# Kernel optimization log

Measured on AMD Instinct MI355X. Metric: run time of the kernel, lower is better.

The kernel has to match this reference:

```python
import jax, jax.numpy as jnp
import numpy as np

B, IN, OUT, E, H, K = 8192, 1024, 256, 16, 512, 3
EPS = 1e-10


def setup_inputs() -> dict:
    key = jax.random.key(0)
    ks = jax.random.split(key, 5)
    scaled = lambda k, shape, fan: jax.random.normal(k, shape, jnp.float32) / np.sqrt(fan)
    return {
        "x": jax.random.normal(ks[0], (B, IN), jnp.float32),
        # torch init is zeros for w_gate (degenerate ties); use small random for a meaningful reference
        "w_gate": jax.random.normal(ks[1], (IN, E), jnp.float32) * 0.02,
        "W1": scaled(ks[2], (E, IN, H), IN),
        "b1": jnp.zeros((E, H), jnp.float32),
        "W2": scaled(ks[3], (E, H, OUT), H),
        "b2": jnp.zeros((E, OUT), jnp.float32),
    }


def _cv_squared(v):
    # torch .var() is unbiased (ddof=1)
    return jnp.var(v, ddof=1) / (jnp.mean(v) ** 2 + EPS)


def reference(x, w_gate, W1, b1, W2, b2):
    # --- top-k gating (eval mode: clean logits, no noise) ---
    logits = x @ w_gate                                   # [B, E]
    top_vals, top_idx = jax.lax.top_k(logits, K)          # [B, K]
    top_gates = jax.nn.softmax(top_vals, axis=-1)         # softmax over selected k
    rows = jnp.arange(logits.shape[0])[:, None]
    gates = jnp.zeros_like(logits).at[rows, top_idx].set(top_gates)  # sparse gates [B, E]

    # --- load-balancing loss ---
    importance = gates.sum(0)
    load = (gates > 0).sum(0).astype(jnp.float32)         # _gates_to_load (eval path)
    loss = _cv_squared(importance) + _cv_squared(load)

    # --- experts (MLP stand-in; dense compute, sparse combine via zero gates) ---
    h = jax.nn.relu(jnp.einsum('bi,eih->beh', x, W1) + b1)  # [B, E, H]
    expert_out = jnp.einsum('beh,eho->beo', h, W2) + b2     # [B, E, OUT]

    # combine: equivalent to SparseDispatcher gather/split/scatter-add with gate weighting
    y = jnp.einsum('be,beo->bo', gates, expert_out)         # [B, OUT]
    return y, loss
```

## Files before the change

kernel.cpp:

```cpp
#include <hip/hip_runtime.h>

#define B_ 8192
#define IN_ 1024
#define OUT_ 256
#define E_ 16
#define KTOP 3
#define H_ 512
#define MAXSLOTS 26624
#define NTILES 208
#define HBLK 16
#define GBLK 2048

typedef __bf16 bf16;
typedef __bf16 bf16x4 __attribute__((ext_vector_type(4)));
typedef __bf16 bf16x8 __attribute__((ext_vector_type(8)));
typedef float f32x4 __attribute__((ext_vector_type(4)));

__device__ __forceinline__ void async16(const bf16* g, bf16* l) {
    __builtin_amdgcn_global_load_lds(
        (const __attribute__((address_space(1))) void*)g,
        (__attribute__((address_space(3))) void*)l,
        16, 0, 0);
}

__global__ __launch_bounds__(256) void k_setup(
    const float* __restrict__ W1, bf16* __restrict__ w1t,
    const float* __restrict__ W2, bf16* __restrict__ w2t,
    int* __restrict__ row_ids, const float* __restrict__ wg, float* __restrict__ wgT,
    bf16* __restrict__ zero_row, int* __restrict__ tile_expert) {
    int bx = blockIdx.x;
    int t = threadIdx.x;
    if (bx >= 2560) {
        if (bx < 2664) {
            row_ids[(bx - 2560) * 256 + t] = -1;
        } else if (bx < 2728) {
            int id = (bx - 2664) * 256 + t;
            int e = id >> 10, j = id & 1023;
            wgT[id] = wg[j * E_ + e];
        } else {
#pragma unroll
            for (int i = 0; i < 4; i++) zero_row[t * 4 + i] = (bf16)0.f;
            if (t < NTILES) tile_expert[t] = -1;
        }
        return;
    }
    __shared__ float tile[64][65];
    const float* in; bf16* out; int Kd, Nd, e, tk, tn;
    if (bx < 2048) {
        in = W1; out = w1t; Kd = IN_; Nd = H_;
        e = bx >> 7; int tt = bx & 127; tk = tt >> 3; tn = tt & 7;
    } else {
        int b2x = bx - 2048;
        in = W2; out = w2t; Kd = H_; Nd = OUT_;
        e = b2x >> 5; int tt = b2x & 31; tk = tt >> 2; tn = tt & 3;
    }
    int r = t >> 6, c = t & 63;
    const float* src = in + ((size_t)e * Kd + tk * 64) * Nd + (size_t)tn * 64;
#pragma unroll
    for (int i = 0; i < 16; i++) {
        int rr = r + i * 4;
        tile[rr][c] = src[(size_t)rr * Nd + c];
    }
    __syncthreads();
    bf16* dst = out + ((size_t)e * Nd + tn * 64) * Kd + (size_t)tk * 64;
#pragma unroll
    for (int i = 0; i < 16; i++) {
        int rr = r + i * 4;
        dst[(size_t)rr * Kd + c] = (bf16)tile[c][rr];
    }
}

__global__ __launch_bounds__(256) void k_gating(
    const float* __restrict__ x, const float* __restrict__ wgT,
    bf16* __restrict__ xbf, int* __restrict__ top_idx, float* __restrict__ top_gate,
    int* __restrict__ partial) {
    __shared__ int lcnt[16];
    int t = threadIdx.x;
    int row = blockIdx.x * 4 + (t >> 6);
    int lane = t & 63;
    if (t < 16) lcnt[t] = 0;
    __syncthreads();
    float acc[16];
#pragma unroll
    for (int e = 0; e < 16; e++) acc[e] = 0.f;
    const float4* x4p = (const float4*)(x + (size_t)row * IN_);
    const float4* w4 = (const float4*)wgT;
#pragma unroll
    for (int it = 0; it < 4; it++) {
        int j0 = it * 64 + lane;
        float4 xv = x4p[j0];
        bf16x4 xb;
        xb[0] = (bf16)xv.x; xb[1] = (bf16)xv.y; xb[2] = (bf16)xv.z; xb[3] = (bf16)xv.w;
        *(bf16x4*)(xbf + (size_t)row * IN_ + j0 * 4) = xb;
#pragma unroll
        for (int e = 0; e < 16; e++) {
            float4 wv = w4[e * 256 + j0];
            acc[e] += xv.x * wv.x + xv.y * wv.y + xv.z * wv.z + xv.w * wv.w;
        }
    }
#pragma unroll
    for (int e = 0; e < 16; e++) {
#pragma unroll
        for (int s = 32; s > 0; s >>= 1) acc[e] += __shfl_xor(acc[e], s, 64);
    }
    if (lane == 0) {
        float v[16];
#pragma unroll
        for (int e = 0; e < 16; e++) v[e] = acc[e];
        int idx[KTOP];
        float val[KTOP];
#pragma unroll
        for (int k = 0; k < KTOP; k++) {
            int best = 0;
            float bv = v[0];
            for (int e = 1; e < 16; e++) {
                if (v[e] > bv) { bv = v[e]; best = e; }
            }
            idx[k] = best; val[k] = bv; v[best] = -1e30f;
        }
        float e1 = __expf(val[1] - val[0]);
        float e2 = __expf(val[2] - val[0]);
        float inv = 1.f / (1.f + e1 + e2);
        float g[KTOP] = {inv, e1 * inv, e2 * inv};
#pragma unroll
        for (int k = 0; k < KTOP; k++) {
            top_idx[row * KTOP + k] = idx[k];
            top_gate[row * KTOP + k] = g[k];
            atomicAdd(&lcnt[idx[k]], 1);
        }
    }
    __syncthreads();
    if (t < 16) partial[blockIdx.x * 16 + t] = lcnt[t];
}

__global__ __launch_bounds__(256) void k_scatterscan(
    const int* __restrict__ top_idx, const float* __restrict__ top_gate,
    const int* __restrict__ partial,
    int* __restrict__ counts, int* __restrict__ tile_expert,
    int* __restrict__ row_ids, int* __restrict__ rowslot,
    float* __restrict__ partial_imp) {
    __shared__ int segsum[16][16];
    __shared__ int tote[16];
    __shared__ int sbase[16];
    __shared__ int lcnt[16];
    __shared__ float limp[16];
    int t = threadIdx.x;
    int blk = blockIdx.x;
    int e = t & 15, seg = t >> 4;
    int s = 0;
    for (int i = 0; i < 128; i++) s += partial[(seg * 128 + i) * 16 + e];
    segsum[seg][e] = s;
    if (t < 16) { lcnt[t] = 0; limp[t] = 0.f; }
    __syncthreads();
    if (t < 16) {
        int total = 0, pre = 0;
        for (int sg = 0; sg < 16; sg++) {
            int v = segsum[sg][t];
            total += v;
            if (sg < blk) pre += v;
        }
        tote[t] = total;
        segsum[0][t] = pre;
    }
    __syncthreads();
    if (t < 16) {
        int off = 0;
        for (int ee = 0; ee < 16; ee++) {
            if (ee == t) break;
            off += (tote[ee] + 127) & ~127;
        }
        sbase[t] = off + segsum[0][t];
        if (blk == 0) {
            counts[t] = tote[t];
            int pd = (tote[t] + 127) & ~127;
            for (int tt = off >> 7; tt < (off + pd) >> 7; ++tt) tile_expert[tt] = t;
        }
    }
    __syncthreads();
#pragma unroll
    for (int j = 0; j < 6; j++) {
        int gid = blk * 1536 + j * 256 + t;
        int ee = top_idx[gid];
        float g = top_gate[gid];
        int rank = atomicAdd(&lcnt[ee], 1);
        atomicAdd(&limp[ee], g);
        int slot = sbase[ee] + rank;
        row_ids[slot] = gid / KTOP;
        rowslot[gid] = slot;
    }
    __syncthreads();
    if (t < 16) partial_imp[blk * 16 + t] = limp[t];
}

__global__ __launch_bounds__(256) void k_gemm1(
    const bf16* __restrict__ xbf, const bf16* __restrict__ w1t,
    const float* __restrict__ b1, const int* __restrict__ row_ids,
    const int* __restrict__ tile_expert, const bf16* __restrict__ zero_row,
    bf16* __restrict__ h) {
    int e = tile_expert[blockIdx.y];
    if (e < 0) return;
    int slot_base = blockIdx.y * 128;
    int nbase = blockIdx.x * 128;
    __shared__ __align__(16) bf16 As[128 * 64];
    __shared__ __align__(16) bf16 Bs[128 * 64];
    int t = threadIdx.x;
    int rmod = (t >> 3) & 7;
    int cglob = (t & 7) ^ rmod;
    const bf16* gA[4];
    const bf16* gB[4];
#pragma unroll
    for (int j = 0; j < 4; j++) {
        int m = j * 32 + (t >> 3);
        int rid = row_ids[slot_base + m];
        gA[j] = ((rid >= 0) ? xbf + (size_t)rid * IN_ : zero_row) + cglob * 8;
        gB[j] = w1t + ((size_t)e * H_ + nbase + m) * IN_ + cglob * 8;
    }
    int w = t >> 6, lane = t & 63;
    int wm = (w >> 1) * 64, wn = (w & 1) * 64;
    int lm = lane & 15, lq = lane >> 4;
    f32x4 acc[4][4] = {};
    for (int k0 = 0; k0 < IN_; k0 += 64) {
#pragma unroll
        for (int j = 0; j < 4; j++) {
            async16(gA[j] + k0, As + (j * 256 + t) * 8);
            async16(gB[j] + k0, Bs + (j * 256 + t) * 8);
        }
        __syncthreads();
        const bf16x8* Av = (const bf16x8*)As;
        const bf16x8* Bv = (const bf16x8*)Bs;
#pragma unroll
        for (int ks = 0; ks < 2; ks++) {
            int kc = ks * 4 + lq;
            bf16x8 af[4], bfv[4];
#pragma unroll
            for (int i = 0; i < 4; i++) {
                int row = wm + i * 16 + lm;
                af[i] = Av[row * 8 + (kc ^ (row & 7))];
            }
#pragma unroll
            for (int i = 0; i < 4; i++) {
                int row = wn + i * 16 + lm;
                bfv[i] = Bv[row * 8 + (kc ^ (row & 7))];
            }
#pragma unroll
            for (int mi = 0; mi < 4; mi++)
#pragma unroll
                for (int ni = 0; ni < 4; ni++)
                    acc[mi][ni] = __builtin_amdgcn_mfma_f32_16x16x32_bf16(af[mi], bfv[ni], acc[mi][ni], 0, 0, 0);
        }
        __syncthreads();
    }
#pragma unroll
    for (int mi = 0; mi < 4; mi++) {
#pragma unroll
        for (int ni = 0; ni < 4; ni++) {
            int colg = nbase + wn + ni * 16 + lm;
            float bias = b1[e * H_ + colg];
#pragma unroll
            for (int r = 0; r < 4; r++) {
                int rowl = wm + mi * 16 + lq * 4 + r;
                float v = acc[mi][ni][r] + bias;
                v = v > 0.f ? v : 0.f;
                h[(size_t)(slot_base + rowl) * H_ + colg] = (bf16)v;
            }
        }
    }
}

__global__ __launch_bounds__(256) void k_gemm2(
    const bf16* __restrict__ h, const bf16* __restrict__ w2t,
    const float* __restrict__ b2, const int* __restrict__ tile_expert,
    bf16* __restrict__ eout) {
    int e = tile_expert[blockIdx.x];
    if (e < 0) return;
    int slot_base = blockIdx.x * 128;
    __shared__ __align__(16) bf16 As[128 * 64];
    __shared__ __align__(16) bf16 Bs[256 * 64];
    int t = threadIdx.x;
    int rmod = (t >> 3) & 7;
    int cglob = (t & 7) ^ rmod;
    const bf16* gA[4];
    const bf16* gB[8];
#pragma unroll
    for (int j = 0; j < 4; j++) {
        int m = j * 32 + (t >> 3);
        gA[j] = h + (size_t)(slot_base + m) * H_ + cglob * 8;
    }
#pragma unroll
    for (int j = 0; j < 8; j++) {
        int m = j * 32 + (t >> 3);
        gB[j] = w2t + ((size_t)e * OUT_ + m) * H_ + cglob * 8;
    }
    int w = t >> 6, lane = t & 63;
    int wm = (w >> 1) * 64, wn = (w & 1) * 128;
    int lm = lane & 15, lq = lane >> 4;
    f32x4 acc[4][8] = {};
    for (int k0 = 0; k0 < H_; k0 += 64) {
#pragma unroll
        for (int j = 0; j < 4; j++) async16(gA[j] + k0, As + (j * 256 + t) * 8);
#pragma unroll
        for (int j = 0; j < 8; j++) async16(gB[j] + k0, Bs + (j * 256 + t) * 8);
        __syncthreads();
        const bf16x8* Av = (const bf16x8*)As;
        const bf16x8* Bv = (const bf16x8*)Bs;
#pragma unroll
        for (int ks = 0; ks < 2; ks++) {
            int kc = ks * 4 + lq;
            bf16x8 af[4], bfv[8];
#pragma unroll
            for (int i = 0; i < 4; i++) {
                int row = wm + i * 16 + lm;
                af[i] = Av[row * 8 + (kc ^ (row & 7))];
            }
#pragma unroll
            for (int i = 0; i < 8; i++) {
                int row = wn + i * 16 + lm;
                bfv[i] = Bv[row * 8 + (kc ^ (row & 7))];
            }
#pragma unroll
            for (int mi = 0; mi < 4; mi++)
#pragma unroll
                for (int ni = 0; ni < 8; ni++)
                    acc[mi][ni] = __builtin_amdgcn_mfma_f32_16x16x32_bf16(af[mi], bfv[ni], acc[mi][ni], 0, 0, 0);
        }
        __syncthreads();
    }
#pragma unroll
    for (int mi = 0; mi < 4; mi++) {
#pragma unroll
        for (int ni = 0; ni < 8; ni++) {
            int colg = wn + ni * 16 + lm;
            float bias = b2[e * OUT_ + colg];
#pragma unroll
            for (int r = 0; r < 4; r++) {
                int rowl = wm + mi * 16 + lq * 4 + r;
                eout[(size_t)(slot_base + rowl) * OUT_ + colg] = (bf16)(acc[mi][ni][r] + bias);
            }
        }
    }
}

__global__ __launch_bounds__(256) void k_combine(
    const bf16* __restrict__ eout, const int* __restrict__ rowslot,
    const float* __restrict__ top_gate, float* __restrict__ y,
    const float* __restrict__ partial_imp, const int* __restrict__ counts,
    float* __restrict__ loss_out) {
    int t = threadIdx.x;
    if (blockIdx.x == B_ / 4) {
        __shared__ float imp[16];
        if (t < 16) {
            float s = 0.f;
#pragma unroll
            for (int b = 0; b < HBLK; b++) s += partial_imp[b * 16 + t];
            imp[t] = s;
        }
        __syncthreads();
        if (t == 0) {
            float si = 0.f, sl = 0.f;
            for (int e = 0; e < E_; e++) { si += imp[e]; sl += (float)counts[e]; }
            float mi_ = si / (float)E_, ml_ = sl / (float)E_;
            float vi = 0.f, vl = 0.f;
            for (int e = 0; e < E_; e++) {
                float d = imp[e] - mi_; vi += d * d;
                float d2 = (float)counts[e] - ml_; vl += d2 * d2;
            }
            vi /= (float)(E_ - 1); vl /= (float)(E_ - 1);
            *loss_out = vi / (mi_ * mi_ + 1e-10f) + vl / (ml_ * ml_ + 1e-10f);
        }
        return;
    }
    int b = blockIdx.x * 4 + (t >> 6);
    int lane = t & 63;
    int s0 = rowslot[b * 3], s1 = rowslot[b * 3 + 1], s2 = rowslot[b * 3 + 2];
    float g0 = top_gate[b * 3], g1 = top_gate[b * 3 + 1], g2 = top_gate[b * 3 + 2];
    bf16x4 v0 = *(const bf16x4*)(eout + (size_t)s0 * OUT_ + lane * 4);
    bf16x4 v1 = *(const bf16x4*)(eout + (size_t)s1 * OUT_ + lane * 4);
    bf16x4 v2 = *(const bf16x4*)(eout + (size_t)s2 * OUT_ + lane * 4);
    float4 r;
    r.x = g0 * (float)v0[0] + g1 * (float)v1[0] + g2 * (float)v2[0];
    r.y = g0 * (float)v0[1] + g1 * (float)v1[1] + g2 * (float)v2[1];
    r.z = g0 * (float)v0[2] + g1 * (float)v1[2] + g2 * (float)v2[2];
    r.w = g0 * (float)v0[3] + g1 * (float)v1[3] + g2 * (float)v2[3];
    ((float4*)y)[(size_t)b * 64 + lane] = r;
}

extern "C" void kernel_launch(void* const* d_in, const int* in_sizes, int n_in,
                              void* d_out, int out_size, void* d_ws, size_t ws_size,
                              hipStream_t stream) {
    (void)in_sizes; (void)n_in; (void)out_size; (void)ws_size;
    const float* x = (const float*)d_in[0];
    const float* wgate = (const float*)d_in[1];
    const float* W1 = (const float*)d_in[2];
    const float* b1 = (const float*)d_in[3];
    const float* W2 = (const float*)d_in[4];
    const float* b2 = (const float*)d_in[5];
    float* y = (float*)d_out;

    char* p = (char*)d_ws;
    auto alloc = [&](size_t bytes) {
        char* q = p;
        p += (bytes + 255) & ~(size_t)255;
        return q;
    };
    bf16* xbf = (bf16*)alloc((size_t)B_ * IN_ * 2);
    bf16* w1t = (bf16*)alloc((size_t)E_ * H_ * IN_ * 2);
    bf16* w2t = (bf16*)alloc((size_t)E_ * OUT_ * H_ * 2);
    bf16* h = (bf16*)alloc((size_t)MAXSLOTS * H_ * 2);
    int* row_ids = (int*)alloc((size_t)MAXSLOTS * 4);
    int* rowslot = (int*)alloc((size_t)B_ * KTOP * 4);
    int* top_idx = (int*)alloc((size_t)B_ * KTOP * 4);
    float* top_gate = (float*)alloc((size_t)B_ * KTOP * 4);
    int* counts = (int*)alloc(E_ * 4);
    int* partial = (int*)alloc((size_t)GBLK * E_ * 4);
    float* partial_imp = (float*)alloc(HBLK * E_ * 4);
    int* tile_expert = (int*)alloc(NTILES * 4);
    bf16* zero_row = (bf16*)alloc(IN_ * 2);
    float* wgT = (float*)alloc((size_t)E_ * IN_ * 4);
    bf16* eout = (bf16*)xbf;

    k_setup<<<dim3(2729), dim3(256), 0, stream>>>(
        W1, w1t, W2, w2t, row_ids, wgate, wgT, zero_row, tile_expert);
    k_gating<<<dim3(GBLK), dim3(256), 0, stream>>>(x, wgT, xbf, top_idx, top_gate, partial);
    k_scatterscan<<<dim3(HBLK), dim3(256), 0, stream>>>(
        top_idx, top_gate, partial, counts, tile_expert, row_ids, rowslot, partial_imp);
    k_gemm1<<<dim3(H_ / 128, NTILES), dim3(256), 0, stream>>>(
        xbf, w1t, b1, row_ids, tile_expert, zero_row, h);
    k_gemm2<<<dim3(NTILES), dim3(256), 0, stream>>>(
        h, w2t, b2, tile_expert, eout);
    k_combine<<<dim3(B_ / 4 + 1), dim3(256), 0, stream>>>(
        eout, rowslot, top_gate, y, partial_imp, counts, y + (size_t)B_ * OUT_);
}
```

Baseline: 212.4 us.

## Fuse MoE pipeline into one persistent kernel with software grid barriers

Replaces the six separate launches (setup, gating, scatter/scan, two expert GEMMs, combine) with a single persistent kernel of 512 blocks. The stages are separated by hand-written atomic grid barriers, plus a tiny kernel that zeroes the barrier counters. Gating now stages w_gate through LDS instead of a pre-transposed copy, and row_ids padding is cleared per expert instead of in full. This is meant to remove launch gaps and tail effects between stages. In exchange it depends on all 512 blocks being co-resident (two per CU) and pays spin-barrier costs, and fewer blocks may underfill the GEMM stages.

Result: slower. 581.2 us (+173.6%).

```diff
diff --git a/kernel.cpp b/kernel.cpp
--- a/kernel.cpp
+++ b/kernel.cpp
@@ -8,8 +8,9 @@
 #define H_ 512
 #define MAXSLOTS 26624
 #define NTILES 208
-#define HBLK 16
-#define GBLK 2048
+#define NBLK 512
+#define GUNITS 2048
+#define P0UNITS 4609
 
 typedef __bf16 bf16;
 typedef __bf16 bf16x4 __attribute__((ext_vector_type(4)));
@@ -23,365 +24,411 @@
         16, 0, 0);
 }
 
-__global__ __launch_bounds__(256) void k_setup(
-    const float* __restrict__ W1, bf16* __restrict__ w1t,
-    const float* __restrict__ W2, bf16* __restrict__ w2t,
-    int* __restrict__ row_ids, const float* __restrict__ wg, float* __restrict__ wgT,
-    bf16* __restrict__ zero_row, int* __restrict__ tile_expert) {
-    int bx = blockIdx.x;
+__global__ void k_zero(int* __restrict__ bar) {
+    for (int i = threadIdx.x; i < 4 * 17 * 32; i += 256) bar[i] = 0;
+}
+
+__device__ __forceinline__ void gbar(int* bar, int b, int blk) {
+    __syncthreads();
+    if (threadIdx.x == 0) {
+        int* base = bar + b * 17 * 32;
+        __threadfence();
+        __hip_atomic_fetch_add(base + (blk & 15) * 32, 1, __ATOMIC_RELEASE, __HIP_MEMORY_SCOPE_AGENT);
+        if (blk == 0) {
+            int sum;
+            do {
+                sum = 0;
+                for (int i = 0; i < 16; i++)
+                    sum += __hip_atomic_load(base + i * 32, __ATOMIC_RELAXED, __HIP_MEMORY_SCOPE_AGENT);
+                if (sum < NBLK) __builtin_amdgcn_s_sleep(8);
+            } while (sum < NBLK);
+            __hip_atomic_store(base + 16 * 32, 1, __ATOMIC_RELEASE, __HIP_MEMORY_SCOPE_AGENT);
+        } else {
+            while (__hip_atomic_load(base + 16 * 32, __ATOMIC_ACQUIRE, __HIP_MEMORY_SCOPE_AGENT) == 0)
+                __builtin_amdgcn_s_sleep(8);
+        }
+        __threadfence();
+    }
+    __syncthreads();
+}
+
+__global__ __launch_bounds__(256, 2) void k_mega(
+    const float* __restrict__ x, const float* __restrict__ wg,
+    const float* __restrict__ W1, const float* __restrict__ b1,
+    const float* __restrict__ W2, const float* __restrict__ b2,
+    bf16* __restrict__ xbf, bf16* __restrict__ w1t, bf16* __restrict__ w2t,
+    bf16* __restrict__ h, bf16* __restrict__ eout,
+    int* __restrict__ row_ids, int* __restrict__ rowslot,
+    int* __restrict__ top_idx, float* __restrict__ top_gate,
+    int* __restrict__ counts, int* __restrict__ partial,
+    float* __restrict__ partial_imp, int* __restrict__ tile_expert,
+    bf16* __restrict__ zero_row, float* __restrict__ y, float* __restrict__ loss_out,
+    int* __restrict__ bar) {
+    __shared__ __align__(16) char smem[49152];
+    int blk = blockIdx.x;
     int t = threadIdx.x;
-    if (bx >= 2560) {
-        if (bx < 2664) {
-            row_ids[(bx - 2560) * 256 + t] = -1;
-        } else if (bx < 2728) {
-            int id = (bx - 2664) * 256 + t;
-            int e = id >> 10, j = id & 1023;
-            wgT[id] = wg[j * E_ + e];
+    int lane = t & 63;
+
+    for (int u = blk; u < P0UNITS; u += NBLK) {
+        if (u < GUNITS) {
+            float4* swg4 = (float4*)smem;
+            int* lcnt = (int*)(smem + 20480);
+            int row = u * 4 + (t >> 6);
+            if (t < 16) lcnt[t] = 0;
+            __syncthreads();
+            float acc[16];
+#pragma unroll
+            for (int e = 0; e < 16; e++) acc[e] = 0.f;
+            const float4* x4p = (const float4*)(x + (size_t)row * IN_);
+            for (int q = 0; q < 4; q++) {
+                const float4* src = (const float4*)(wg + q * 4096);
+#pragma unroll
+                for (int i = 0; i < 4; i++) {
+                    int f = i * 256 + t;
+                    swg4[(f >> 2) * 5 + (f & 3)] = src[f];
+                }
+                __syncthreads();
+                float4 xv = x4p[q * 64 + lane];
+                bf16x4 xb;
+                xb[0] = (bf16)xv.x; xb[1] = (bf16)xv.y; xb[2] = (bf16)xv.z; xb[3] = (bf16)xv.w;
+                *(bf16x4*)(xbf + (size_t)row * IN_ + (q * 64 + lane) * 4) = xb;
+                float xs[4] = {xv.x, xv.y, xv.z, xv.w};
+#pragma unroll
+                for (int i = 0; i < 4; i++) {
+                    int r = lane * 4 + i;
+#pragma unroll
+                    for (int e4 = 0; e4 < 4; e4++) {
+                        float4 wv = swg4[r * 5 + e4];
+                        acc[e4 * 4 + 0] += xs[i] * wv.x;
+                        acc[e4 * 4 + 1] += xs[i] * wv.y;
+                        acc[e4 * 4 + 2] += xs[i] * wv.z;
+                        acc[e4 * 4 + 3] += xs[i] * wv.w;
+                    }
+                }
+                __syncthreads();
+            }
+#pragma unroll
+            for (int e = 0; e < 16; e++) {
+#pragma unroll
+                for (int s = 32; s > 0; s >>= 1) acc[e] += __shfl_xor(acc[e], s, 64);
+            }
+            if (lane == 0) {
+                float v[16];
+#pragma unroll
+                for (int e = 0; e < 16; e++) v[e] = acc[e];
+                int idx[KTOP];
+                float val[KTOP];
+#pragma unroll
+                for (int k = 0; k < KTOP; k++) {
+                    int best = 0;
+                    float bv = v[0];
+                    for (int e = 1; e < 16; e++) {
+                        if (v[e] > bv) { bv = v[e]; best = e; }
+                    }
+                    idx[k] = best; val[k] = bv; v[best] = -1e30f;
+                }
+                float e1 = __expf(val[1] - val[0]);
+                float e2 = __expf(val[2] - val[0]);
+                float inv = 1.f / (1.f + e1 + e2);
+                float g[KTOP] = {inv, e1 * inv, e2 * inv};
+#pragma unroll
+                for (int k = 0; k < KTOP; k++) {
+                    top_idx[row * KTOP + k] = idx[k];
+                    top_gate[row * KTOP + k] = g[k];
+                    atomicAdd(&lcnt[idx[k]], 1);
+                }
+            }
+            __syncthreads();
+            if (t < 16) partial[u * 16 + t] = lcnt[t];
+        } else if (u < 4608) {
+            __syncthreads();
+            float (*tile)[65] = (float(*)[65])smem;
+            const float* in; bf16* out; int Kd, Nd, e, tk, tn;
+            if (u < 4096) {
+                int b1x = u - 2048;
+                in = W1; out = w1t; Kd = IN_; Nd = H_;
+                e = b1x >> 7; int tt = b1x & 127; tk = tt >> 3; tn = tt & 7;
+            } else {
+                int b2x = u - 4096;
+                in = W2; out = w2t; Kd = H_; Nd = OUT_;
+                e = b2x >> 5; int tt = b2x & 31; tk = tt >> 2; tn = tt & 3;
+            }
+            int r = t >> 6, c = t & 63;
+            const float* src = in + ((size_t)e * Kd + tk * 64) * Nd + (size_t)tn * 64;
+#pragma unroll
+            for (int i = 0; i < 16; i++) {
+                int rr = r + i * 4;
+                tile[rr][c] = src[(size_t)rr * Nd + c];
+            }
+            __syncthreads();
+            bf16* dst = out + ((size_t)e * Nd + tn * 64) * Kd + (size_t)tk * 64;
+#pragma unroll
+            for (int i = 0; i < 16; i++) {
+                int rr = r + i * 4;
+                dst[(size_t)rr * Kd + c] = (bf16)tile[c][rr];
+            }
         } else {
 #pragma unroll
             for (int i = 0; i < 4; i++) zero_row[t * 4 + i] = (bf16)0.f;
-            if (t < NTILES) tile_expert[t] = -1;
-        }
-        return;
-    }
-    __shared__ float tile[64][65];
-    const float* in; bf16* out; int Kd, Nd, e, tk, tn;
-    if (bx < 2048) {
-        in = W1; out = w1t; Kd = IN_; Nd = H_;
-        e = bx >> 7; int tt = bx & 127; tk = tt >> 3; tn = tt & 7;
-    } else {
-        int b2x = bx - 2048;
-        in = W2; out = w2t; Kd = H_; Nd = OUT_;
-        e = b2x >> 5; int tt = b2x & 31; tk = tt >> 2; tn = tt & 3;
-    }
-    int r = t >> 6, c = t & 63;
-    const float* src = in + ((size_t)e * Kd + tk * 64) * Nd + (size_t)tn * 64;
-#pragma unroll
-    for (int i = 0; i < 16; i++) {
-        int rr = r + i * 4;
-        tile[rr][c] = src[(size_t)rr * Nd + c];
-    }
-    __syncthreads();
-    bf16* dst = out + ((size_t)e * Nd + tn * 64) * Kd + (size_t)tk * 64;
-#pragma unroll
-    for (int i = 0; i < 16; i++) {
-        int rr = r + i * 4;
-        dst[(size_t)rr * Kd + c] = (bf16)tile[c][rr];
-    }
-}
-
-__global__ __launch_bounds__(256) void k_gating(
-    const float* __restrict__ x, const float* __restrict__ wgT,
-    bf16* __restrict__ xbf, int* __restrict__ top_idx, float* __restrict__ top_gate,
-    int* __restrict__ partial) {
-    __shared__ int lcnt[16];
-    int t = threadIdx.x;
-    int row = blockIdx.x * 4 + (t >> 6);
-    int lane = t & 63;
-    if (t < 16) lcnt[t] = 0;
-    __syncthreads();
-    float acc[16];
-#pragma unroll
-    for (int e = 0; e < 16; e++) acc[e] = 0.f;
-    const float4* x4p = (const float4*)(x + (size_t)row * IN_);
-    const float4* w4 = (const float4*)wgT;
-#pragma unroll
-    for (int it = 0; it < 4; it++) {
-        int j0 = it * 64 + lane;
-        float4 xv = x4p[j0];
-        bf16x4 xb;
-        xb[0] = (bf16)xv.x; xb[1] = (bf16)xv.y; xb[2] = (bf16)xv.z; xb[3] = (bf16)xv.w;
-        *(bf16x4*)(xbf + (size_t)row * IN_ + j0 * 4) = xb;
-#pragma unroll
-        for (int e = 0; e < 16; e++) {
-            float4 wv = w4[e * 256 + j0];
-            acc[e] += xv.x * wv.x + xv.y * wv.y + xv.z * wv.z + xv.w * wv.w;
-        }
-    }
-#pragma unroll
-    for (int e = 0; e < 16; e++) {
-#pragma unroll
-        for (int s = 32; s > 0; s >>= 1) acc[e] += __shfl_xor(acc[e], s, 64);
-    }
-    if (lane == 0) {
-        float v[16];
-#pragma unroll
-        for (int e = 0; e < 16; e++) v[e] = acc[e];
-        int idx[KTOP];
-        float val[KTOP];
-#pragma unroll
-        for (int k = 0; k < KTOP; k++) {
-            int best = 0;
-            float bv = v[0];
-            for (int e = 1; e < 16; e++) {
-                if (v[e] > bv) { bv = v[e]; best = e; }
-            }
-            idx[k] = best; val[k] = bv; v[best] = -1e30f;
-        }
-        float e1 = __expf(val[1] - val[0]);
-        float e2 = __expf(val[2] - val[0]);
-        float inv = 1.f / (1.f + e1 + e2);
-        float g[KTOP] = {inv, e1 * inv, e2 * inv};
-#pragma unroll
-        for (int k = 0; k < KTOP; k++) {
-            top_idx[row * KTOP + k] = idx[k];
-            top_gate[row * KTOP + k] = g[k];
-            atomicAdd(&lcnt[idx[k]], 1);
-        }
-    }
-    __syncthreads();
-    if (t < 16) partial[blockIdx.x * 16 + t] = lcnt[t];
-}
-
-__global__ __launch_bounds__(256) void k_scatterscan(
-    const int* __restrict__ top_idx, const float* __restrict__ top_gate,
-    const int* __restrict__ partial,
-    int* __restrict__ counts, int* __restrict__ tile_expert,
-    int* __restrict__ row_ids, int* __restrict__ rowslot,
-    float* __restrict__ partial_imp) {
-    __shared__ int segsum[16][16];
-    __shared__ int tote[16];
-    __shared__ int sbase[16];
-    __shared__ int lcnt[16];
-    __shared__ float limp[16];
-    int t = threadIdx.x;
-    int blk = blockIdx.x;
-    int e = t & 15, seg = t >> 4;
-    int s = 0;
-    for (int i = 0; i < 128; i++) s += partial[(seg * 128 + i) * 16 + e];
-    segsum[seg][e] = s;
-    if (t < 16) { lcnt[t] = 0; limp[t] = 0.f; }
-    __syncthreads();
-    if (t < 16) {
-        int total = 0, pre = 0;
-        for (int sg = 0; sg < 16; sg++) {
-            int v = segsum[sg][t];
-            total += v;
-            if (sg < blk) pre += v;
-        }
-        tote[t] = total;
-        segsum[0][t] = pre;
-    }
-    __syncthreads();
-    if (t < 16) {
-        int off = 0;
-        for (int ee = 0; ee < 16; ee++) {
-            if (ee == t) break;
-            off += (tote[ee] + 127) & ~127;
-        }
-        sbase[t] = off + segsum[0][t];
+        }
+    }
+    gbar(bar, 0, blk);
+
+    if (blk < 16) {
+        struct SS {
+            int segsum[16][16];
+            int tote[16], spre[16], soff[16], lcnt[16];
+            float limp[16];
+        };
+        SS* ss = (SS*)smem;
+        int e = t & 15, seg = t >> 4;
+        int s = 0;
+        for (int i = 0; i < 128; i++) s += partial[(seg * 128 + i) * 16 + e];
+        ss->segsum[seg][e] = s;
+        if (t < 16) { ss->lcnt[t] = 0; ss->limp[t] = 0.f; }
+        __syncthreads();
+        if (t < 16) {
+            int total = 0, pre = 0;
+            for (int sg = 0; sg < 16; sg++) {
+                int v = ss->segsum[sg][t];
+                total += v;
+                if (sg < blk) pre += v;
+            }
+            ss->tote[t] = total;
+            ss->spre[t] = pre;
+        }
+        __syncthreads();
+        if (t < 16) {
+            int off = 0;
+            for (int ee = 0; ee < t; ee++) off += (ss->tote[ee] + 127) & ~127;
+            ss->soff[t] = off;
+            if (blk == 0) counts[t] = ss->tote[t];
+        }
+        __syncthreads();
         if (blk == 0) {
-            counts[t] = tote[t];
-            int pd = (tote[t] + 127) & ~127;
-            for (int tt = off >> 7; tt < (off + pd) >> 7; ++tt) tile_expert[tt] = t;
-        }
-    }
-    __syncthreads();
-#pragma unroll
-    for (int j = 0; j < 6; j++) {
-        int gid = blk * 1536 + j * 256 + t;
-        int ee = top_idx[gid];
-        float g = top_gate[gid];
-        int rank = atomicAdd(&lcnt[ee], 1);
-        atomicAdd(&limp[ee], g);
-        int slot = sbase[ee] + rank;
-        row_ids[slot] = gid / KTOP;
-        rowslot[gid] = slot;
-    }
-    __syncthreads();
-    if (t < 16) partial_imp[blk * 16 + t] = limp[t];
-}
-
-__global__ __launch_bounds__(256) void k_gemm1(
-    const bf16* __restrict__ xbf, const bf16* __restrict__ w1t,
-    const float* __restrict__ b1, const int* __restrict__ row_ids,
-    const int* __restrict__ tile_expert, const bf16* __restrict__ zero_row,
-    bf16* __restrict__ h) {
-    int e = tile_expert[blockIdx.y];
-    if (e < 0) return;
-    int slot_base = blockIdx.y * 128;
-    int nbase = blockIdx.x * 128;
-    __shared__ __align__(16) bf16 As[128 * 64];
-    __shared__ __align__(16) bf16 Bs[128 * 64];
-    int t = threadIdx.x;
-    int rmod = (t >> 3) & 7;
-    int cglob = (t & 7) ^ rmod;
-    const bf16* gA[4];
-    const bf16* gB[4];
-#pragma unroll
-    for (int j = 0; j < 4; j++) {
-        int m = j * 32 + (t >> 3);
-        int rid = row_ids[slot_base + m];
-        gA[j] = ((rid >= 0) ? xbf + (size_t)rid * IN_ : zero_row) + cglob * 8;
-        gB[j] = w1t + ((size_t)e * H_ + nbase + m) * IN_ + cglob * 8;
-    }
-    int w = t >> 6, lane = t & 63;
-    int wm = (w >> 1) * 64, wn = (w & 1) * 64;
-    int lm = lane & 15, lq = lane >> 4;
-    f32x4 acc[4][4] = {};
-    for (int k0 = 0; k0 < IN_; k0 += 64) {
-#pragma unroll
-        for (int j = 0; j < 4; j++) {
-            async16(gA[j] + k0, As + (j * 256 + t) * 8);
-            async16(gB[j] + k0, Bs + (j * 256 + t) * 8);
+            if (t < 16) {
+                int off = ss->soff[t], pd = (ss->tote[t] + 127) & ~127;
+                for (int tt = off >> 7; tt < (off + pd) >> 7; ++tt) tile_expert[tt] = t;
+            }
+            if (t == 0) {
+                int tot = ss->soff[15] + ((ss->tote[15] + 127) & ~127);
+                for (int tt = tot >> 7; tt < NTILES; ++tt) tile_expert[tt] = -1;
+            }
+        }
+        {
+            int pb = ss->soff[blk] + ss->tote[blk];
+            int pe = ss->soff[blk] + ((ss->tote[blk] + 127) & ~127);
+            for (int i = pb + t; i < pe; i += 256) row_ids[i] = -1;
+        }
+#pragma unroll
+        for (int j = 0; j < 6; j++) {
+            int gid = blk * 1536 + j * 256 + t;
+            int ee = top_idx[gid];
+            float g = top_gate[gid];
+            int rank = atomicAdd(&ss->lcnt[ee], 1);
+            atomicAdd(&ss->limp[ee], g);
+            int slot = ss->soff[ee] + ss->spre[ee] + rank;
+            row_ids[slot] = gid / KTOP;
+            rowslot[gid] = slot;
         }
         __syncthreads();
-        const bf16x8* Av = (const bf16x8*)As;
-        const bf16x8* Bv = (const bf16x8*)Bs;
-#pragma unroll
-        for (int ks = 0; ks < 2; ks++) {
-            int kc = ks * 4 + lq;
-            bf16x8 af[4], bfv[4];
-#pragma unroll
-            for (int i = 0; i < 4; i++) {
-                int row = wm + i * 16 + lm;
-                af[i] = Av[row * 8 + (kc ^ (row & 7))];
-            }
-#pragma unroll
-            for (int i = 0; i < 4; i++) {
-                int row = wn + i * 16 + lm;
-                bfv[i] = Bv[row * 8 + (kc ^ (row & 7))];
-            }
-#pragma unroll
-            for (int mi = 0; mi < 4; mi++)
-#pragma unroll
-                for (int ni = 0; ni < 4; ni++)
-                    acc[mi][ni] = __builtin_amdgcn_mfma_f32_16x16x32_bf16(af[mi], bfv[ni], acc[mi][ni], 0, 0, 0);
-        }
-        __syncthreads();
-    }
-#pragma unroll
-    for (int mi = 0; mi < 4; mi++) {
-#pragma unroll
-        for (int ni = 0; ni < 4; ni++) {
-            int colg = nbase + wn + ni * 16 + lm;
-            float bias = b1[e * H_ + colg];
-#pragma unroll
-            for (int r = 0; r < 4; r++) {
-                int rowl = wm + mi * 16 + lq * 4 + r;
-                float v = acc[mi][ni][r] + bias;
-                v = v > 0.f ? v : 0.f;
-                h[(size_t)(slot_base + rowl) * H_ + colg] = (bf16)v;
-            }
-        }
-    }
-}
-
-__global__ __launch_bounds__(256) void k_gemm2(
-    const bf16* __restrict__ h, const bf16* __restrict__ w2t,
-    const float* __restrict__ b2, const int* __restrict__ tile_expert,
-    bf16* __restrict__ eout) {
-    int e = tile_expert[blockIdx.x];
-    if (e < 0) return;
-    int slot_base = blockIdx.x * 128;
-    __shared__ __align__(16) bf16 As[128 * 64];
-    __shared__ __align__(16) bf16 Bs[256 * 64];
-    int t = threadIdx.x;
-    int rmod = (t >> 3) & 7;
-    int cglob = (t & 7) ^ rmod;
-    const bf16* gA[4];
-    const bf16* gB[8];
-#pragma unroll
-    for (int j = 0; j < 4; j++) {
-        int m = j * 32 + (t >> 3);
-        gA[j] = h + (size_t)(slot_base + m) * H_ + cglob * 8;
-    }
-#pragma unroll
-    for (int j = 0; j < 8; j++) {
-        int m = j * 32 + (t >> 3);
-        gB[j] = w2t + ((size_t)e * OUT_ + m) * H_ + cglob * 8;
-    }
-    int w = t >> 6, lane = t & 63;
-    int wm = (w >> 1) * 64, wn = (w & 1) * 128;
-    int lm = lane & 15, lq = lane >> 4;
-    f32x4 acc[4][8] = {};
-    for (int k0 = 0; k0 < H_; k0 += 64) {
-#pragma unroll
-        for (int j = 0; j < 4; j++) async16(gA[j] + k0, As + (j * 256 + t) * 8);
-#pragma unroll
-        for (int j = 0; j < 8; j++) async16(gB[j] + k0, Bs + (j * 256 + t) * 8);
-        __syncthreads();
-        const bf16x8* Av = (const bf16x8*)As;
-        const bf16x8* Bv = (const bf16x8*)Bs;
-#pragma unroll
-        for (int ks = 0; ks < 2; ks++) {
-            int kc = ks * 4 + lq;
-            bf16x8 af[4], bfv[8];
-#pragma unroll
-            for (int i = 0; i < 4; i++) {
-                int row = wm + i * 16 + lm;
-                af[i] = Av[row * 8 + (kc ^ (row & 7))];
-            }
-#pragma unroll
-            for (int i = 0; i < 8; i++) {
-                int row = wn + i * 16 + lm;
-                bfv[i] = Bv[row * 8 + (kc ^ (row & 7))];
-            }
-#pragma unroll
-            for (int mi = 0; mi < 4; mi++)
-#pragma unroll
-                for (int ni = 0; ni < 8; ni++)
-                    acc[mi][ni] = __builtin_amdgcn_mfma_f32_16x16x32_bf16(af[mi], bfv[ni], acc[mi][ni], 0, 0, 0);
-        }
-        __syncthreads();
-    }
-#pragma unroll
-    for (int mi = 0; mi < 4; mi++) {
-#pragma unroll
-        for (int ni = 0; ni < 8; ni++) {
-            int colg = wn + ni * 16 + lm;
-            float bias = b2[e * OUT_ + colg];
-#pragma unroll
-            for (int r = 0; r < 4; r++) {
-                int rowl = wm + mi * 16 + lq * 4 + r;
-                eout[(size_t)(slot_base + rowl) * OUT_ + colg] = (bf16)(acc[mi][ni][r] + bias);
-            }
-        }
-    }
-}
-
-__global__ __launch_bounds__(256) void k_combine(
-    const bf16* __restrict__ eout, const int* __restrict__ rowslot,
-    const float* __restrict__ top_gate, float* __restrict__ y,
-    const float* __restrict__ partial_imp, const int* __restrict__ counts,
-    float* __restrict__ loss_out) {
-    int t = threadIdx.x;
-    if (blockIdx.x == B_ / 4) {
-        __shared__ float imp[16];
-        if (t < 16) {
-            float s = 0.f;
-#pragma unroll
-            for (int b = 0; b < HBLK; b++) s += partial_imp[b * 16 + t];
-            imp[t] = s;
-        }
-        __syncthreads();
-        if (t == 0) {
-            float si = 0.f, sl = 0.f;
-            for (int e = 0; e < E_; e++) { si += imp[e]; sl += (float)counts[e]; }
-            float mi_ = si / (float)E_, ml_ = sl / (float)E_;
-            float vi = 0.f, vl = 0.f;
-            for (int e = 0; e < E_; e++) {
-                float d = imp[e] - mi_; vi += d * d;
-                float d2 = (float)counts[e] - ml_; vl += d2 * d2;
-            }
-            vi /= (float)(E_ - 1); vl /= (float)(E_ - 1);
-            *loss_out = vi / (mi_ * mi_ + 1e-10f) + vl / (ml_ * ml_ + 1e-10f);
-        }
-        return;
-    }
-    int b = blockIdx.x * 4 + (t >> 6);
-    int lane = t & 63;
-    int s0 = rowslot[b * 3], s1 = rowslot[b * 3 + 1], s2 = rowslot[b * 3 + 2];
-    float g0 = top_gate[b * 3], g1 = top_gate[b * 3 + 1], g2 = top_gate[b * 3 + 2];
-    bf16x4 v0 = *(const bf16x4*)(eout + (size_t)s0 * OUT_ + lane * 4);
-    bf16x4 v1 = *(const bf16x4*)(eout + (size_t)s1 * OUT_ + lane * 4);
-    bf16x4 v2 = *(const bf16x4*)(eout + (size_t)s2 * OUT_ + lane * 4);
-    float4 r;
-    r.x = g0 * (float)v0[0] + g1 * (float)v1[0] + g2 * (float)v2[0];
-    r.y = g0 * (float)v0[1] + g1 * (float)v1[1] + g2 * (float)v2[1];
-    r.z = g0 * (float)v0[2] + g1 * (float)v1[2] + g2 * (float)v2[2];
-    r.w = g0 * (float)v0[3] + g1 * (float)v1[3] + g2 * (float)v2[3];
-    ((float4*)y)[(size_t)b * 64 + lane] = r;
+        if (t < 16) partial_imp[blk * 16 + t] = ss->limp[t];
+    }
+    gbar(bar, 1, blk);
+
+    {
+        bf16* As = (bf16*)smem;
+        bf16* Bs = (bf16*)(smem + 16384);
+        int w = t >> 6;
+        int wm = (w >> 1) * 64, wn = (w & 1) * 64;
+        int lm = lane & 15, lq = lane >> 4;
+        int rmod = (t >> 3) & 7;
+        int cglob = (t & 7) ^ rmod;
+        for (int u = blk; u < 832; u += NBLK) {
+            int tilei = u >> 2;
+            int e = tile_expert[tilei];
+            if (e < 0) continue;
+            int slot_base = tilei * 128;
+            int nbase = (u & 3) * 128;
+            const bf16* gA[4];
+            const bf16* gB[4];
+#pragma unroll
+            for (int j = 0; j < 4; j++) {
+                int m = j * 32 + (t >> 3);
+                int rid = row_ids[slot_base + m];
+                gA[j] = ((rid >= 0) ? xbf + (size_t)rid * IN_ : zero_row) + cglob * 8;
+                gB[j] = w1t + ((size_t)e * H_ + nbase + m) * IN_ + cglob * 8;
+            }
+            f32x4 acc[4][4] = {};
+            for (int k0 = 0; k0 < IN_; k0 += 64) {
+#pragma unroll
+                for (int j = 0; j < 4; j++) {
+                    async16(gA[j] + k0, As + (j * 256 + t) * 8);
+                    async16(gB[j] + k0, Bs + (j * 256 + t) * 8);
+                }
+                __syncthreads();
+                const bf16x8* Av = (const bf16x8*)As;
+                const bf16x8* Bv = (const bf16x8*)Bs;
+#pragma unroll
+                for (int ks = 0; ks < 2; ks++) {
+                    int kc = ks * 4 + lq;
+                    bf16x8 af[4], bfv[4];
+#pragma unroll
+                    for (int i = 0; i < 4; i++) {
+                        int row = wm + i * 16 + lm;
+                        af[i] = Av[row * 8 + (kc ^ (row & 7))];
+                    }
+#pragma unroll
+                    for (int i = 0; i < 4; i++) {
+                        int row = wn + i * 16 + lm;
+                        bfv[i] = Bv[row * 8 + (kc ^ (row & 7))];
+                    }
+#pragma unroll
+                    for (int mi = 0; mi < 4; mi++)
+#pragma unroll
+                        for (int ni = 0; ni < 4; ni++)
+                            acc[mi][ni] = __builtin_amdgcn_mfma_f32_16x16x32_bf16(af[mi], bfv[ni], acc[mi][ni], 0, 0, 0);
+                }
+                __syncthreads();
+            }
+#pragma unroll
+            for (int mi = 0; mi < 4; mi++) {
+#pragma unroll
+                for (int ni = 0; ni < 4; ni++) {
+                    int colg = nbase + wn + ni * 16 + lm;
+                    float bias = b1[e * H_ + colg];
+#pragma unroll
+                    for (int r = 0; r < 4; r++) {
+                        int rowl = wm + mi * 16 + lq * 4 + r;
+                        float v = acc[mi][ni][r] + bias;
+                        v = v > 0.f ? v : 0.f;
+                        h[(size_t)(slot_base + rowl) * H_ + colg] = (bf16)v;
+                    }
+                }
+            }
+        }
+    }
+    gbar(bar, 2, blk);
+
+    {
+        bf16* As = (bf16*)smem;
+        bf16* Bs = (bf16*)(smem + 16384);
+        int w = t >> 6;
+        int wm = (w >> 1) * 64, wn = (w & 1) * 128;
+        int lm = lane & 15, lq = lane >> 4;
+        int rmod = (t >> 3) & 7;
+        int cglob = (t & 7) ^ rmod;
+        for (int u = blk; u < NTILES; u += NBLK) {
+            int e = tile_expert[u];
+            if (e < 0) continue;
+            int slot_base = u * 128;
+            const bf16* gA[4];
+            const bf16* gB[8];
+#pragma unroll
+            for (int j = 0; j < 4; j++) {
+                int m = j * 32 + (t >> 3);
+                gA[j] = h + (size_t)(slot_base + m) * H_ + cglob * 8;
+            }
+#pragma unroll
+            for (int j = 0; j < 8; j++) {
+                int m = j * 32 + (t >> 3);
+                gB[j] = w2t + ((size_t)e * OUT_ + m) * H_ + cglob * 8;
+            }
+            f32x4 acc[4][8] = {};
+            for (int k0 = 0; k0 < H_; k0 += 64) {
+#pragma unroll
+                for (int j = 0; j < 4; j++) async16(gA[j] + k0, As + (j * 256 + t) * 8);
+#pragma unroll
+                for (int j = 0; j < 8; j++) async16(gB[j] + k0, Bs + (j * 256 + t) * 8);
+                __syncthreads();
+                const bf16x8* Av = (const bf16x8*)As;
+                const bf16x8* Bv = (const bf16x8*)Bs;
+#pragma unroll
+                for (int ks = 0; ks < 2; ks++) {
+                    int kc = ks * 4 + lq;
+                    bf16x8 af[4], bfv[8];
+#pragma unroll
+                    for (int i = 0; i < 4; i++) {
+                        int row = wm + i * 16 + lm;
+                        af[i] = Av[row * 8 + (kc ^ (row & 7))];
+                    }
+#pragma unroll
+                    for (int i = 0; i < 8; i++) {
+                        int row = wn + i * 16 + lm;
+                        bfv[i] = Bv[row * 8 + (kc ^ (row & 7))];
+                    }
+#pragma unroll
+                    for (int mi = 0; mi < 4; mi++)
+#pragma unroll
+                        for (int ni = 0; ni < 8; ni++)
+                            acc[mi][ni] = __builtin_amdgcn_mfma_f32_16x16x32_bf16(af[mi], bfv[ni], acc[mi][ni], 0, 0, 0);
+                }
+                __syncthreads();
+            }
+#pragma unroll
+            for (int mi = 0; mi < 4; mi++) {
+#pragma unroll
+                for (int ni = 0; ni < 8; ni++) {
+                    int colg = wn + ni * 16 + lm;
+                    float bias = b2[e * OUT_ + colg];
+#pragma unroll
+                    for (int r = 0; r < 4; r++) {
+                        int rowl = wm + mi * 16 + lq * 4 + r;
+                        eout[(size_t)(slot_base + rowl) * OUT_ + colg] = (bf16)(acc[mi][ni][r] + bias);
+                    }
+                }
+            }
+        }
+    }
+    gbar(bar, 3, blk);
+
+    for (int u = blk; u < B_ / 4 + 1; u += NBLK) {
+        if (u == B_ / 4) {
+            float* imp = (float*)smem;
+            if (t < 16) {
+                float s = 0.f;
+#pragma unroll
+                for (int b = 0; b < 16; b++) s += partial_imp[b * 16 + t];
+                imp[t] = s;
+            }
+            __syncthreads();
+            if (t == 0) {
+                float si = 0.f, sl = 0.f;
+                for (int e = 0; e < E_; e++) { si += imp[e]; sl += (float)counts[e]; }
+                float mi_ = si / (float)E_, ml_ = sl / (float)E_;
+                float vi = 0.f, vl = 0.f;
+                for (int e = 0; e < E_; e++) {
+                    float d = imp[e] - mi_; vi += d * d;
+                    float d2 = (float)counts[e] - ml_; vl += d2 * d2;
+                }
+                vi /= (float)(E_ - 1); vl /= (float)(E_ - 1);
+                *loss_out = vi / (mi_ * mi_ + 1e-10f) + vl / (ml_ * ml_ + 1e-10f);
+            }
+            __syncthreads();
+            continue;
+        }
+        int b = u * 4 + (t >> 6);
+        int s0 = rowslot[b * 3], s1 = rowslot[b * 3 + 1], s2 = rowslot[b * 3 + 2];
+        float g0 = top_gate[b * 3], g1 = top_gate[b * 3 + 1], g2 = top_gate[b * 3 + 2];
+        unsigned long long r0 = __hip_atomic_load(
+            (const unsigned long long*)(eout + (size_t)s0 * OUT_ + lane * 4),
+            __ATOMIC_RELAXED, __HIP_MEMORY_SCOPE_AGENT);
+        unsigned long long r1 = __hip_atomic_load(
+            (const unsigned long long*)(eout + (size_t)s1 * OUT_ + lane * 4),
+            __ATOMIC_RELAXED, __HIP_MEMORY_SCOPE_AGENT);
+        unsigned long long r2 = __hip_atomic_load(
+            (const unsigned long long*)(eout + (size_t)s2 * OUT_ + lane * 4),
+            __ATOMIC_RELAXED, __HIP_MEMORY_SCOPE_AGENT);
+        bf16x4 v0 = *(bf16x4*)&r0;
+        bf16x4 v1 = *(bf16x4*)&r1;
+        bf16x4 v2 = *(bf16x4*)&r2;
+        float4 r;
+        r.x = g0 * (float)v0[0] + g1 * (float)v1[0] + g2 * (float)v2[0];
+        r.y = g0 * (float)v0[1] + g1 * (float)v1[1] + g2 * (float)v2[1];
+        r.z = g0 * (float)v0[2] + g1 * (float)v1[2] + g2 * (float)v2[2];
+        r.w = g0 * (float)v0[3] + g1 * (float)v1[3] + g2 * (float)v2[3];
+        ((float4*)y)[(size_t)b * 64 + lane] = r;
+    }
 }
 
 extern "C" void kernel_launch(void* const* d_in, const int* in_sizes, int n_in,
@@ -411,22 +458,16 @@
     int* top_idx = (int*)alloc((size_t)B_ * KTOP * 4);
     float* top_gate = (float*)alloc((size_t)B_ * KTOP * 4);
     int* counts = (int*)alloc(E_ * 4);
-    int* partial = (int*)alloc((size_t)GBLK * E_ * 4);
-    float* partial_imp = (float*)alloc(HBLK * E_ * 4);
+    int* partial = (int*)alloc((size_t)GUNITS * E_ * 4);
+    float* partial_imp = (float*)alloc(16 * E_ * 4);
     int* tile_expert = (int*)alloc(NTILES * 4);
     bf16* zero_row = (bf16*)alloc(IN_ * 2);
-    float* wgT = (float*)alloc((size_t)E_ * IN_ * 4);
+    int* bar = (int*)alloc(4 * 17 * 32 * 4);
     bf16* eout = (bf16*)xbf;
 
-    k_setup<<<dim3(2729), dim3(256), 0, stream>>>(
-        W1, w1t, W2, w2t, row_ids, wgate, wgT, zero_row, tile_expert);
-    k_gating<<<dim3(GBLK), dim3(256), 0, stream>>>(x, wgT, xbf, top_idx, top_gate, partial);
-    k_scatterscan<<<dim3(HBLK), dim3(256), 0, stream>>>(
-        top_idx, top_gate, partial, counts, tile_expert, row_ids, rowslot, partial_imp);
-    k_gemm1<<<dim3(H_ / 128, NTILES), dim3(256), 0, stream>>>(
-        xbf, w1t, b1, row_ids, tile_expert, zero_row, h);
-    k_gemm2<<<dim3(NTILES), dim3(256), 0, stream>>>(
-        h, w2t, b2, tile_expert, eout);
-    k_combine<<<dim3(B_ / 4 + 1), dim3(256), 0, stream>>>(
-        eout, rowslot, top_gate, y, partial_imp, counts, y + (size_t)B_ * OUT_);
+    k_zero<<<dim3(1), dim3(256), 0, stream>>>(bar);
+    k_mega<<<dim3(NBLK), dim3(256), 0, stream>>>(
+        x, wgate, W1, b1, W2, b2, xbf, w1t, w2t, h, eout,
+        row_ids, rowslot, top_idx, top_gate, counts, partial, partial_imp,
+        tile_expert, zero_row, y, y + (size_t)B_ * OUT_, bar);
 }
```

## Fuse gating into setup kernel and stage gate weights through LDS

Applied to the files above, without the earlier changes.

Merges the weight-transpose setup kernel and the gating kernel into one launch so that gating blocks and weight-conversion blocks can run concurrently. The gating path no longer needs a pre-transposed wgT buffer. Each block instead stages chunks of w_gate into padded shared memory and accumulates the per-lane partial dot products from there. This removes one kernel launch and the dependency between the two stages. In exchange it adds extra syncthreads, repeated w_gate reads per block, and a larger shared-memory footprint that may lower occupancy.

Result: no change. 211.2 us (-0.5%).

```diff
diff --git a/kernel.cpp b/kernel.cpp
--- a/kernel.cpp
+++ b/kernel.cpp
@@ -23,20 +23,91 @@
         16, 0, 0);
 }
 
-__global__ __launch_bounds__(256) void k_setup(
-    const float* __restrict__ W1, bf16* __restrict__ w1t,
-    const float* __restrict__ W2, bf16* __restrict__ w2t,
-    int* __restrict__ row_ids, const float* __restrict__ wg, float* __restrict__ wgT,
-    bf16* __restrict__ zero_row, int* __restrict__ tile_expert) {
+__global__ __launch_bounds__(256) void k_stage1(
+    const float* __restrict__ x, const float* __restrict__ wg,
+    const float* __restrict__ W1, const float* __restrict__ W2,
+    bf16* __restrict__ xbf, int* __restrict__ top_idx, float* __restrict__ top_gate,
+    int* __restrict__ partial,
+    bf16* __restrict__ w1t, bf16* __restrict__ w2t,
+    int* __restrict__ row_ids, bf16* __restrict__ zero_row, int* __restrict__ tile_expert) {
+    __shared__ __align__(16) float smem[5140];
     int bx = blockIdx.x;
     int t = threadIdx.x;
-    if (bx >= 2560) {
-        if (bx < 2664) {
-            row_ids[(bx - 2560) * 256 + t] = -1;
-        } else if (bx < 2728) {
-            int id = (bx - 2664) * 256 + t;
-            int e = id >> 10, j = id & 1023;
-            wgT[id] = wg[j * E_ + e];
+    if (bx < GBLK) {
+        int* lcnt = (int*)(smem + 5124);
+        int lane = t & 63;
+        int row = bx * 4 + (t >> 6);
+        if (t < 16) lcnt[t] = 0;
+        float acc[16];
+#pragma unroll
+        for (int e = 0; e < 16; e++) acc[e] = 0.f;
+        const float4* x4p = (const float4*)(x + (size_t)row * IN_);
+        float4* swg4 = (float4*)smem;
+        for (int q = 0; q < 4; q++) {
+            const float4* src = (const float4*)(wg + q * 4096);
+#pragma unroll
+            for (int i = 0; i < 4; i++) {
+                int f = i * 256 + t;
+                swg4[(f >> 2) * 5 + (f & 3)] = src[f];
+            }
+            __syncthreads();
+            float4 xv = x4p[q * 64 + lane];
+            bf16x4 xb;
+            xb[0] = (bf16)xv.x; xb[1] = (bf16)xv.y; xb[2] = (bf16)xv.z; xb[3] = (bf16)xv.w;
+            *(bf16x4*)(xbf + (size_t)row * IN_ + (q * 64 + lane) * 4) = xb;
+            float xs[4] = {xv.x, xv.y, xv.z, xv.w};
+#pragma unroll
+            for (int i = 0; i < 4; i++) {
+                int r = lane * 4 + i;
+#pragma unroll
+                for (int e4 = 0; e4 < 4; e4++) {
+                    float4 wv = swg4[r * 5 + e4];
+                    acc[e4 * 4 + 0] += xs[i] * wv.x;
+                    acc[e4 * 4 + 1] += xs[i] * wv.y;
+                    acc[e4 * 4 + 2] += xs[i] * wv.z;
+                    acc[e4 * 4 + 3] += xs[i] * wv.w;
+                }
+            }
+            __syncthreads();
+        }
+#pragma unroll
+        for (int e = 0; e < 16; e++) {
+#pragma unroll
+            for (int s = 32; s > 0; s >>= 1) acc[e] += __shfl_xor(acc[e], s, 64);
+        }
+        if (lane == 0) {
+            float v[16];
+#pragma unroll
+            for (int e = 0; e < 16; e++) v[e] = acc[e];
+            int idx[KTOP];
+            float val[KTOP];
+#pragma unroll
+            for (int k = 0; k < KTOP; k++) {
+                int best = 0;
+                float bv = v[0];
+                for (int e = 1; e < 16; e++) {
+                    if (v[e] > bv) { bv = v[e]; best = e; }
+                }
+                idx[k] = best; val[k] = bv; v[best] = -1e30f;
+            }
+            float e1 = __expf(val[1] - val[0]);
+            float e2 = __expf(val[2] - val[0]);
+            float inv = 1.f / (1.f + e1 + e2);
+            float g[KTOP] = {inv, e1 * inv, e2 * inv};
+#pragma unroll
+            for (int k = 0; k < KTOP; k++) {
+                top_idx[row * KTOP + k] = idx[k];
+                top_gate[row * KTOP + k] = g[k];
+                atomicAdd(&lcnt[idx[k]], 1);
+            }
+        }
+        __syncthreads();
+        if (t < 16) partial[bx * 16 + t] = lcnt[t];
+        return;
+    }
+    if (bx >= 4608) {
+        if (bx < 4712) {
+            row_ids[(bx - 4608) * 256 + t] = -1;
         } else {
 #pragma unroll
             for (int i = 0; i < 4; i++) zero_row[t * 4 + i] = (bf16)0.f;
@@ -44,13 +115,14 @@
         }
         return;
     }
-    __shared__ float tile[64][65];
+    float (*tile)[65] = (float(*)[65])smem;
     const float* in; bf16* out; int Kd, Nd, e, tk, tn;
-    if (bx < 2048) {
+    if (bx < 4096) {
+        int b1x = bx - 2048;
         in = W1; out = w1t; Kd = IN_; Nd = H_;
-        e = bx >> 7; int tt = bx & 127; tk = tt >> 3; tn = tt & 7;
+        e = b1x >> 7; int tt = b1x & 127; tk = tt >> 3; tn = tt & 7;
     } else {
-        int b2x = bx - 2048;
+        int b2x = bx - 4096;
         in = W2; out = w2t; Kd = H_; Nd = OUT_;
         e = b2x >> 5; int tt = b2x & 31; tk = tt >> 2; tn = tt & 3;
     }
@@ -68,69 +140,6 @@
         int rr = r + i * 4;
         dst[(size_t)rr * Kd + c] = (bf16)tile[c][rr];
     }
-}
-
-__global__ __launch_bounds__(256) void k_gating(
-    const float* __restrict__ x, const float* __restrict__ wgT,
-    bf16* __restrict__ xbf, int* __restrict__ top_idx, float* __restrict__ top_gate,
-    int* __restrict__ partial) {
-    __shared__ int lcnt[16];
-    int t = threadIdx.x;
-    int row = blockIdx.x * 4 + (t >> 6);
-    int lane = t & 63;
-    if (t < 16) lcnt[t] = 0;
-    __syncthreads();
-    float acc[16];
-#pragma unroll
-    for (int e = 0; e < 16; e++) acc[e] = 0.f;
-    const float4* x4p = (const float4*)(x + (size_t)row * IN_);
-    const float4* w4 = (const float4*)wgT;
-#pragma unroll
-    for (int it = 0; it < 4; it++) {
-        int j0 = it * 64 + lane;
-        float4 xv = x4p[j0];
-        bf16x4 xb;
-        xb[0] = (bf16)xv.x; xb[1] = (bf16)xv.y; xb[2] = (bf16)xv.z; xb[3] = (bf16)xv.w;
-        *(bf16x4*)(xbf + (size_t)row * IN_ + j0 * 4) = xb;
-#pragma unroll
-        for (int e = 0; e < 16; e++) {
-            float4 wv = w4[e * 256 + j0];
-            acc[e] += xv.x * wv.x + xv.y * wv.y + xv.z * wv.z + xv.w * wv.w;
-        }
-    }
-#pragma unroll
-    for (int e = 0; e < 16; e++) {
-#pragma unroll
-        for (int s = 32; s > 0; s >>= 1) acc[e] += __shfl_xor(acc[e], s, 64);
-    }
-    if (lane == 0) {
-        float v[16];
-#pragma unroll
-        for (int e = 0; e < 16; e++) v[e] = acc[e];
-        int idx[KTOP];
-        float val[KTOP];
-#pragma unroll
-        for (int k = 0; k < KTOP; k++) {
-            int best = 0;
-            float bv = v[0];
-            for (int e = 1; e < 16; e++) {
-                if (v[e] > bv) { bv = v[e]; best = e; }
-            }
-            idx[k] = best; val[k] = bv; v[best] = -1e30f;
-        }
-        float e1 = __expf(val[1] - val[0]);
-        float e2 = __expf(val[2] - val[0]);
-        float inv = 1.f / (1.f + e1 + e2);
-        float g[KTOP] = {inv, e1 * inv, e2 * inv};
-#pragma unroll
-        for (int k = 0; k < KTOP; k++) {
-            top_idx[row * KTOP + k] = idx[k];
-            top_gate[row * KTOP + k] = g[k];
-            atomicAdd(&lcnt[idx[k]], 1);
-        }
-    }
-    __syncthreads();
-    if (t < 16) partial[blockIdx.x * 16 + t] = lcnt[t];
 }
 
 __global__ __launch_bounds__(256) void k_scatterscan(
@@ -415,12 +424,11 @@
     float* partial_imp = (float*)alloc(HBLK * E_ * 4);
     int* tile_expert = (int*)alloc(NTILES * 4);
     bf16* zero_row = (bf16*)alloc(IN_ * 2);
-    float* wgT = (float*)alloc((size_t)E_ * IN_ * 4);
     bf16* eout = (bf16*)xbf;
 
-    k_setup<<<dim3(2729), dim3(256), 0, stream>>>(
-        W1, w1t, W2, w2t, row_ids, wgate, wgT, zero_row, tile_expert);
-    k_gating<<<dim3(GBLK), dim3(256), 0, stream>>>(x, wgT, xbf, top_idx, top_gate, partial);
+    k_stage1<<<dim3(4713), dim3(256), 0, stream>>>(
+        x, wgate, W1, W2, xbf, top_idx, top_gate, partial, w1t, w2t,
+        row_ids, zero_row, tile_expert);
     k_scatterscan<<<dim3(HBLK), dim3(256), 0, stream>>>(
         top_idx, top_gate, partial, counts, tile_expert, row_ids, rowslot, partial_imp);
     k_gemm1<<<dim3(H_ / 128, NTILES), dim3(256), 0, stream>>>(
```
